# Kernel optimization log

Measured on AMD Instinct MI355X. Metric: run time of the kernel, lower is better.

## Reference

```python
import jax, jax.numpy as jnp
import numpy as np

B, H, W, C = 4, 64, 64, 256
DQK = C // 16  # query/key channels = 16


def setup_inputs() -> dict:
    key = jax.random.key(0)
    ks = jax.random.split(key, 8)
    s = 0.05
    return {
        "x": jax.random.normal(ks[0], (B, H, W, C), dtype=jnp.float32),
        "wq": jax.random.normal(ks[1], (C, DQK), dtype=jnp.float32) * s,
        "bq": jax.random.normal(ks[2], (DQK,), dtype=jnp.float32) * s,
        "wk": jax.random.normal(ks[3], (C, DQK), dtype=jnp.float32) * s,
        "bk": jax.random.normal(ks[4], (DQK,), dtype=jnp.float32) * s,
        "wv": jax.random.normal(ks[5], (C, C), dtype=jnp.float32) * s,
        "bv": jax.random.normal(ks[6], (C,), dtype=jnp.float32) * s,
        "gamma": jax.random.normal(ks[7], (), dtype=jnp.float32),
    }


def reference(x, wq, bq, wk, bk, wv, bv, gamma):
    # 1x1 convs == per-pixel linear projections
    q = jnp.einsum('bhwc,cd->bhwd', x, wq) + bq          # [B,H,W,DQK]
    k = jnp.einsum('bhwc,cd->bhwd', x, wk) + bk          # [B,H,W,DQK]
    v = jnp.einsum('bhwc,cd->bhwd', x, wv) + bv          # [B,H,W,C]
    hw = H * W
    q = q.reshape(B, hw, DQK)
    k = k.reshape(B, hw, DQK)
    v = v.reshape(B, hw, C)
    energy = jnp.einsum('bnd,bmd->bnm', q, k)            # [B,HW,HW]
    attention = jax.nn.softmax(energy, axis=-1)
    out = jnp.einsum('bnm,bmc->bnc', attention, v)       # [B,HW,C]
    out = out.reshape(B, H, W, C)
    return out * gamma + x, attention
```

## Files before the change

kernel.cpp:

```cpp
#include <hip/hip_runtime.h>

typedef _Float16 half8 __attribute__((ext_vector_type(8)));
typedef _Float16 half4v __attribute__((ext_vector_type(4)));
typedef __fp16 fp16x2 __attribute__((ext_vector_type(2)));
typedef float f32x16 __attribute__((ext_vector_type(16)));
typedef float f32x4 __attribute__((ext_vector_type(4)));
typedef unsigned int uint2v __attribute__((ext_vector_type(2)));

#define MFMA16(a, b, c) __builtin_amdgcn_mfma_f32_32x32x16_f16((a), (b), (c), 0, 0, 0)
#define QSC 1.44269504088896f

#define OFF_WB   0
#define OFF_WQK  131072
#define OFF_QF   147456
#define OFF_KF   671744
#define OFF_VB   1196032
#define OFF_MLP  9584640

__device__ inline unsigned int pkf16(float a, float b) {
    union { fp16x2 h; unsigned int u; } cv;
    cv.h = __builtin_amdgcn_cvt_pkrtz(a, b);
    return cv.u;
}
__device__ inline half8 mk8(unsigned int w0, unsigned int w1, unsigned int w2, unsigned int w3) {
    union { unsigned int u[4]; half8 h; } cv;
    cv.u[0] = w0; cv.u[1] = w1; cv.u[2] = w2; cv.u[3] = w3; return cv.h;
}

__global__ __launch_bounds__(256) void k_prep(const float* __restrict__ wq,
                                              const float* __restrict__ wk,
                                              const float* __restrict__ wv,
                                              _Float16* __restrict__ WB,
                                              _Float16* __restrict__ WQK) {
    int idx = blockIdx.x * 256 + threadIdx.x;
    if (idx < 65536) {
        int j = idx & 7, l = (idx >> 3) & 63, kc = idx >> 12;
        int ct = (idx >> 9) & 7;
        int k = kc * 16 + (l >> 5) * 8 + j;
        int c = ct * 32 + (l & 31);
        WB[idx] = (_Float16)wv[k * 256 + c];
    } else if (idx < 65536 + 8192) {
        int t = idx - 65536;
        int j = t & 7, l = (t >> 3) & 63, kc = t >> 9;
        int k = kc * 16 + (l >> 5) * 8 + j;
        int c = l & 31;
        WQK[t] = (_Float16)((c < 16) ? wq[k * 16 + c] : wk[k * 16 + (c - 16)]);
    }
}

__global__ __launch_bounds__(256, 2) void k_proj(const float* __restrict__ x,
                                                 const float* __restrict__ bq,
                                                 const float* __restrict__ bk,
                                                 const float* __restrict__ bv,
                                                 const _Float16* __restrict__ WB,
                                                 const _Float16* __restrict__ WQK,
                                                 _Float16* __restrict__ Qf,
                                                 _Float16* __restrict__ Kf,
                                                 _Float16* __restrict__ VB) {
    const int tid = threadIdx.x;
    const int w = tid >> 6, l = tid & 63, lo = l & 31, h = l >> 5;
    const long rowbase = (long)blockIdx.x * 32;
    const float* xp = x + (rowbase + lo) * 256 + h * 8;

    f32x16 acc0 = {}, acc1 = {}, accQK = {};
#pragma unroll
    for (int kc = 0; kc < 16; ++kc) {
        float4 a0 = *(const float4*)(xp + kc * 16);
        float4 a1 = *(const float4*)(xp + kc * 16 + 4);
        half8 xf;
        xf[0] = (_Float16)a0.x; xf[1] = (_Float16)a0.y; xf[2] = (_Float16)a0.z; xf[3] = (_Float16)a0.w;
        xf[4] = (_Float16)a1.x; xf[5] = (_Float16)a1.y; xf[6] = (_Float16)a1.z; xf[7] = (_Float16)a1.w;
        half8 b0 = *(const half8*)(WB + ((kc * 8 + 2 * w) * 64 + l) * 8);
        half8 b1 = *(const half8*)(WB + ((kc * 8 + 2 * w + 1) * 64 + l) * 8);
        acc0 = MFMA16(xf, b0, acc0);
        acc1 = MFMA16(xf, b1, acc1);
        if (w == 0) {
            half8 bqk = *(const half8*)(WQK + (kc * 64 + l) * 8);
            accQK = MFMA16(xf, bqk, accQK);
        }
    }

    const int b = (int)(rowbase >> 12);
    const int k16base = (int)((rowbase & 4095) >> 4);
#pragma unroll
    for (int cti = 0; cti < 2; ++cti) {
        int ct = 2 * w + cti;
        f32x16 acc = cti ? acc1 : acc0;
        float bias = bv[ct * 32 + lo];
#pragma unroll
        for (int g = 0; g < 4; ++g) {
            int K16 = k16base + (g >> 1);
            int lanep = (g & 1) * 32 + lo;
            _Float16* dst = VB + ((((long)b * 256 + K16) * 8 + ct) * 64 + lanep) * 8 + 4 * h;
            half4v pv;
            pv[0] = (_Float16)(acc[4 * g + 0] + bias);
            pv[1] = (_Float16)(acc[4 * g + 1] + bias);
            pv[2] = (_Float16)(acc[4 * g + 2] + bias);
            pv[3] = (_Float16)(acc[4 * g + 3] + bias);
            *(half4v*)dst = pv;
        }
    }
    if (w == 0) {
        float bias = (lo < 16) ? bq[lo] : bk[lo - 16];
#pragma unroll
        for (int r = 0; r < 16; ++r) {
            int kl = (r & 3) + 8 * (r >> 2) + 4 * h;
            long n = rowbase + kl;
            float v = accQK[r] + bias;
            if (lo < 16) Qf[n * 16 + lo] = (_Float16)(v * QSC);
            else         Kf[n * 16 + (lo - 16)] = (_Float16)v;
        }
    }
}

__global__ __launch_bounds__(256, 4) void k_ml(const _Float16* __restrict__ Qf,
                                               const _Float16* __restrict__ Kf,
                                               float2* __restrict__ MLp) {
    const int bid = blockIdx.x;
    const int kh = bid & 1;
    const int qi = bid >> 1;
    const int b = qi >> 7, qt = qi & 127;
    const int tid = threadIdx.x, w = tid >> 6, l = tid & 63, lo = l & 31, h = l >> 5;
    const int qbase = qt * 32;

    half8 qf = *(const half8*)(Qf + (((long)b * 4096 + qbase + lo) << 4) + h * 8);
    const _Float16* Kb = Kf + ((long)b * 4096 << 4);

    float m = -3e38f, lsum = 0.f;
    for (int i = 0; i < 16; ++i) {
        int t = kh * 64 + i * 4 + w;
        half8 kf = *(const half8*)(Kb + ((t * 32 + lo) << 4) + h * 8);
        f32x16 e = MFMA16(kf, qf, (f32x16){});
        float t0 = fmaxf(fmaxf(e[0], e[1]), fmaxf(e[2], e[3]));
        float t1 = fmaxf(fmaxf(e[4], e[5]), fmaxf(e[6], e[7]));
        float t2 = fmaxf(fmaxf(e[8], e[9]), fmaxf(e[10], e[11]));
        float t3 = fmaxf(fmaxf(e[12], e[13]), fmaxf(e[14], e[15]));
        float tmax = fmaxf(fmaxf(t0, t1), fmaxf(t2, t3));
        tmax = fmaxf(tmax, __shfl_xor(tmax, 32));
        if (tmax > m) { lsum *= exp2f(m - tmax); m = tmax; }
        float ss = 0.f;
#pragma unroll
        for (int r = 0; r < 16; ++r) ss += exp2f(e[r] - m);
        lsum += ss;
    }
    lsum += __shfl_xor(lsum, 32);

    __shared__ float sm[4][32];
    __shared__ float sl[4][32];
    if (l < 32) { sm[w][lo] = m; sl[w][lo] = lsum; }
    __syncthreads();
    if (tid < 32) {
        float M = fmaxf(fmaxf(sm[0][tid], sm[1][tid]), fmaxf(sm[2][tid], sm[3][tid]));
        float L = sl[0][tid] * exp2f(sm[0][tid] - M) + sl[1][tid] * exp2f(sm[1][tid] - M) +
                  sl[2][tid] * exp2f(sm[2][tid] - M) + sl[3][tid] * exp2f(sm[3][tid] - M);
        float2 v; v.x = M; v.y = L;
        MLp[(((long)b * 4096 + qbase + tid) << 1) + kh] = v;
    }
}

__global__ __launch_bounds__(256, 4) void k_attn(const float* __restrict__ x,
                                                 const float* __restrict__ gptr,
                                                 const _Float16* __restrict__ Qf,
                                                 const _Float16* __restrict__ Kf,
                                                 const _Float16* __restrict__ VB,
                                                 const float2* __restrict__ MLp,
                                                 float* __restrict__ out0,
                                                 float* __restrict__ attn) {
    const int bid = blockIdx.x;
    const int sp = bid & 1;
    const int qt = (bid >> 1) & 127;
    const int b  = bid >> 8;
    const int tid = threadIdx.x, w = tid >> 6, l = tid & 63, lo = l & 31, h = l >> 5;
    const int qbase = qt * 32;

    half8 qf = *(const half8*)(Qf + (((long)b * 4096 + qbase + lo) << 4) + h * 8);
    const _Float16* Kb = Kf + ((long)b * 4096 << 4);

    const float2* mlrow = MLp + ((long)(b * 4096 + qbase + lo) << 1);
    float2 mla = mlrow[0];
    float2 mlc = mlrow[1];
    float Mrow = fmaxf(mla.x, mlc.x);
    const float S_lane = Mrow + __log2f(mla.y * exp2f(mla.x - Mrow) + mlc.y * exp2f(mlc.x - Mrow));

    const _Float16* vb = VB + (long)b * 256 * 8 * 64 * 8;

    __shared__ float ldsS[32 * 132];

    const int srow = tid >> 3;
    const int st7 = tid & 7;
    float* aout = attn + (long)b * 4096 * 4096 + ((long)(qbase + srow) << 12) + st7 * 4;

    f32x16 oacc[4] = {};

    for (int i = 0; i < 32; ++i) {
        int t = i * 4 + w;
        half8 kf = *(const half8*)(Kb + ((t * 32 + lo) << 4) + h * 8);
        f32x16 e = MFMA16(kf, qf, (f32x16){});
        float p[16];
#pragma unroll
        for (int r = 0; r < 16; ++r) p[r] = exp2f(e[r] - S_lane);

        if ((i >> 4) == sp) {
            __syncthreads();
#pragma unroll
            for (int g = 0; g < 4; ++g) {
                f32x4 st = { p[4 * g + 0], p[4 * g + 1], p[4 * g + 2], p[4 * g + 3] };
                *(f32x4*)&ldsS[lo * 132 + w * 32 + g * 8 + h * 4] = st;
            }
            __syncthreads();
            float* ap = aout + i * 128;
#pragma unroll
            for (int seg = 0; seg < 4; ++seg) {
                f32x4 v = *(const f32x4*)&ldsS[srow * 132 + seg * 32 + st7 * 4];
                *(f32x4*)(ap + seg * 32) = v;
            }
        }

        unsigned int u0 = pkf16(p[0], p[1]),   x0 = pkf16(p[4], p[5]);
        unsigned int v0 = pkf16(p[2], p[3]),   y0 = pkf16(p[6], p[7]);
        unsigned int u1 = pkf16(p[8], p[9]),   x1 = pkf16(p[12], p[13]);
        unsigned int v1 = pkf16(p[10], p[11]), y1 = pkf16(p[14], p[15]);
        uint2v t0 = __builtin_amdgcn_permlane32_swap(u0, x0, false, false);
        uint2v t1 = __builtin_amdgcn_permlane32_swap(v0, y0, false, false);
        uint2v t2 = __builtin_amdgcn_permlane32_swap(u1, x1, false, false);
        uint2v t3 = __builtin_amdgcn_permlane32_swap(v1, y1, false, false);
        half8 pa0 = mk8(t0.x, t1.x, t0.y, t1.y);
        half8 pa1 = mk8(t2.x, t3.x, t2.y, t3.y);

#pragma unroll
        for (int ct = 0; ct < 4; ++ct) {
            int ctg = 4 * sp + ct;
            half8 vf0 = *(const half8*)(vb + (((long)(2 * t + 0) * 8 + ctg) * 64 + l) * 8);
            half8 vf1 = *(const half8*)(vb + (((long)(2 * t + 1) * 8 + ctg) * 64 + l) * 8);
            oacc[ct] = MFMA16(pa0, vf0, oacc[ct]);
            oacc[ct] = MFMA16(pa1, vf1, oacc[ct]);
        }
    }

#pragma unroll 1
    for (int ww = 0; ww < 4; ++ww) {
        __syncthreads();
        if (w == ww) {
#pragma unroll
            for (int ct = 0; ct < 4; ++ct) {
#pragma unroll
                for (int r = 0; r < 16; ++r) {
                    int row = (r & 3) + 8 * (r >> 2) + 4 * h;
                    float val = oacc[ct][r];
                    if (ww == 0) ldsS[row * 132 + ct * 32 + lo] = val;
                    else         ldsS[row * 132 + ct * 32 + lo] += val;
                }
            }
        }
    }
    __syncthreads();

    float gamma = *gptr;
    int cb = st7 << 4;
    long base = ((long)b * 4096 + qbase + srow) * 256 + sp * 128 + cb;
    const float* xp = x + base;
    float* op = out0 + base;
#pragma unroll
    for (int c0 = 0; c0 < 16; c0 += 4) {
        float4 xv = *(const float4*)(xp + c0);
        f32x4 ov;
        ov.x = gamma * ldsS[srow * 132 + cb + c0 + 0] + xv.x;
        ov.y = gamma * ldsS[srow * 132 + cb + c0 + 1] + xv.y;
        ov.z = gamma * ldsS[srow * 132 + cb + c0 + 2] + xv.z;
        ov.w = gamma * ldsS[srow * 132 + cb + c0 + 3] + xv.w;
        *(f32x4*)(op + c0) = ov;
    }
}

extern "C" void kernel_launch(void* const* d_in, const int* in_sizes, int n_in,
                              void* d_out, int out_size, void* d_ws, size_t ws_size,
                              hipStream_t stream) {
    const float* x  = (const float*)d_in[0];
    const float* wq = (const float*)d_in[1];
    const float* bq = (const float*)d_in[2];
    const float* wk = (const float*)d_in[3];
    const float* bk = (const float*)d_in[4];
    const float* wv = (const float*)d_in[5];
    const float* bv = (const float*)d_in[6];
    const float* gamma = (const float*)d_in[7];

    char* ws = (char*)d_ws;
    _Float16* WB  = (_Float16*)(ws + OFF_WB);
    _Float16* WQK = (_Float16*)(ws + OFF_WQK);
    _Float16* Qf  = (_Float16*)(ws + OFF_QF);
    _Float16* Kf  = (_Float16*)(ws + OFF_KF);
    _Float16* VB  = (_Float16*)(ws + OFF_VB);
    float2*   MLp = (float2*)(ws + OFF_MLP);

    float* out0 = (float*)d_out;
    float* attn = (float*)d_out + 4194304;

    k_prep<<<288, 256, 0, stream>>>(wq, wk, wv, WB, WQK);
    k_proj<<<512, 256, 0, stream>>>(x, bq, bk, bv, WB, WQK, Qf, Kf, VB);
    k_ml  <<<1024, 256, 0, stream>>>(Qf, Kf, MLp);
    k_attn<<<1024, 256, 0, stream>>>(x, gamma, Qf, Kf, VB, MLp, out0, attn);
}
```

Baseline: 144.7 us.

## Fuse softmax stats with PV into one kernel, split attention-matrix write into own kernel

Merges the max/sum pass and the P·V accumulation into a single kernel. Each block now covers all keys and all 256 output channels for 32 queries. It writes the log-sum-exp per row to workspace instead of partial (max, sum) pairs. The large fp32 attention-matrix store moves to a separate, high-occupancy kernel that recomputes QK^T and exp and streams rows out. This separates the compute-heavy PV work from the bandwidth-bound write so each kernel can be shaped for its own bottleneck, at the cost of a third QK^T evaluation, fewer blocks in the PV kernel (512 with 8 accumulators) and lower occupancy there.

```diff
diff --git a/kernel.cpp b/kernel.cpp
--- a/kernel.cpp
+++ b/kernel.cpp
@@ -15,7 +15,7 @@
 #define OFF_QF   147456
 #define OFF_KF   671744
 #define OFF_VB   1196032
-#define OFF_MLP  9584640
+#define OFF_S    9584640
 
 __device__ inline unsigned int pkf16(float a, float b) {
     union { fp16x2 h; unsigned int u; } cv;
@@ -113,13 +113,15 @@
     }
 }
 
-__global__ __launch_bounds__(256, 4) void k_ml(const _Float16* __restrict__ Qf,
-                                               const _Float16* __restrict__ Kf,
-                                               float2* __restrict__ MLp) {
+__global__ __launch_bounds__(256, 2) void k_mlpv(const float* __restrict__ x,
+                                                 const float* __restrict__ gptr,
+                                                 const _Float16* __restrict__ Qf,
+                                                 const _Float16* __restrict__ Kf,
+                                                 const _Float16* __restrict__ VB,
+                                                 float* __restrict__ Sg,
+                                                 float* __restrict__ out0) {
     const int bid = blockIdx.x;
-    const int kh = bid & 1;
-    const int qi = bid >> 1;
-    const int b = qi >> 7, qt = qi & 127;
+    const int b = bid >> 7, qt = bid & 127;
     const int tid = threadIdx.x, w = tid >> 6, l = tid & 63, lo = l & 31, h = l >> 5;
     const int qbase = qt * 32;
 
@@ -127,8 +129,8 @@
     const _Float16* Kb = Kf + ((long)b * 4096 << 4);
 
     float m = -3e38f, lsum = 0.f;
-    for (int i = 0; i < 16; ++i) {
-        int t = kh * 64 + i * 4 + w;
+    for (int i = 0; i < 32; ++i) {
+        int t = i * 4 + w;
         half8 kf = *(const half8*)(Kb + ((t * 32 + lo) << 4) + h * 8);
         f32x16 e = MFMA16(kf, qf, (f32x16){});
         float t0 = fmaxf(fmaxf(e[0], e[1]), fmaxf(e[2], e[3]));
@@ -149,48 +151,19 @@
     __shared__ float sl[4][32];
     if (l < 32) { sm[w][lo] = m; sl[w][lo] = lsum; }
     __syncthreads();
+    float M = fmaxf(fmaxf(sm[0][lo], sm[1][lo]), fmaxf(sm[2][lo], sm[3][lo]));
+    float L = sl[0][lo] * exp2f(sm[0][lo] - M) + sl[1][lo] * exp2f(sm[1][lo] - M) +
+              sl[2][lo] * exp2f(sm[2][lo] - M) + sl[3][lo] * exp2f(sm[3][lo] - M);
+    const float S_lane = M + __log2f(L);
     if (tid < 32) {
-        float M = fmaxf(fmaxf(sm[0][tid], sm[1][tid]), fmaxf(sm[2][tid], sm[3][tid]));
-        float L = sl[0][tid] * exp2f(sm[0][tid] - M) + sl[1][tid] * exp2f(sm[1][tid] - M) +
-                  sl[2][tid] * exp2f(sm[2][tid] - M) + sl[3][tid] * exp2f(sm[3][tid] - M);
-        float2 v; v.x = M; v.y = L;
-        MLp[(((long)b * 4096 + qbase + tid) << 1) + kh] = v;
-    }
-}
-
-__global__ __launch_bounds__(256, 4) void k_attn(const float* __restrict__ x,
-                                                 const float* __restrict__ gptr,
-                                                 const _Float16* __restrict__ Qf,
-                                                 const _Float16* __restrict__ Kf,
-                                                 const _Float16* __restrict__ VB,
-                                                 const float2* __restrict__ MLp,
-                                                 float* __restrict__ out0,
-                                                 float* __restrict__ attn) {
-    const int bid = blockIdx.x;
-    const int sp = bid & 1;
-    const int qt = (bid >> 1) & 127;
-    const int b  = bid >> 8;
-    const int tid = threadIdx.x, w = tid >> 6, l = tid & 63, lo = l & 31, h = l >> 5;
-    const int qbase = qt * 32;
-
-    half8 qf = *(const half8*)(Qf + (((long)b * 4096 + qbase + lo) << 4) + h * 8);
-    const _Float16* Kb = Kf + ((long)b * 4096 << 4);
-
-    const float2* mlrow = MLp + ((long)(b * 4096 + qbase + lo) << 1);
-    float2 mla = mlrow[0];
-    float2 mlc = mlrow[1];
-    float Mrow = fmaxf(mla.x, mlc.x);
-    const float S_lane = Mrow + __log2f(mla.y * exp2f(mla.x - Mrow) + mlc.y * exp2f(mlc.x - Mrow));
+        float Mr = fmaxf(fmaxf(sm[0][tid], sm[1][tid]), fmaxf(sm[2][tid], sm[3][tid]));
+        float Lr = sl[0][tid] * exp2f(sm[0][tid] - Mr) + sl[1][tid] * exp2f(sm[1][tid] - Mr) +
+                   sl[2][tid] * exp2f(sm[2][tid] - Mr) + sl[3][tid] * exp2f(sm[3][tid] - Mr);
+        Sg[b * 4096 + qbase + tid] = Mr + __log2f(Lr);
+    }
 
     const _Float16* vb = VB + (long)b * 256 * 8 * 64 * 8;
-
-    __shared__ float ldsS[32 * 132];
-
-    const int srow = tid >> 3;
-    const int st7 = tid & 7;
-    float* aout = attn + (long)b * 4096 * 4096 + ((long)(qbase + srow) << 12) + st7 * 4;
-
-    f32x16 oacc[4] = {};
+    f32x16 oacc[8] = {};
 
     for (int i = 0; i < 32; ++i) {
         int t = i * 4 + w;
@@ -199,22 +172,6 @@
         float p[16];
 #pragma unroll
         for (int r = 0; r < 16; ++r) p[r] = exp2f(e[r] - S_lane);
-
-        if ((i >> 4) == sp) {
-            __syncthreads();
-#pragma unroll
-            for (int g = 0; g < 4; ++g) {
-                f32x4 st = { p[4 * g + 0], p[4 * g + 1], p[4 * g + 2], p[4 * g + 3] };
-                *(f32x4*)&ldsS[lo * 132 + w * 32 + g * 8 + h * 4] = st;
-            }
-            __syncthreads();
-            float* ap = aout + i * 128;
-#pragma unroll
-            for (int seg = 0; seg < 4; ++seg) {
-                f32x4 v = *(const f32x4*)&ldsS[srow * 132 + seg * 32 + st7 * 4];
-                *(f32x4*)(ap + seg * 32) = v;
-            }
-        }
 
         unsigned int u0 = pkf16(p[0], p[1]),   x0 = pkf16(p[4], p[5]);
         unsigned int v0 = pkf16(p[2], p[3]),   y0 = pkf16(p[6], p[7]);
@@ -228,27 +185,27 @@
         half8 pa1 = mk8(t2.x, t3.x, t2.y, t3.y);
 
 #pragma unroll
-        for (int ct = 0; ct < 4; ++ct) {
-            int ctg = 4 * sp + ct;
-            half8 vf0 = *(const half8*)(vb + (((long)(2 * t + 0) * 8 + ctg) * 64 + l) * 8);
-            half8 vf1 = *(const half8*)(vb + (((long)(2 * t + 1) * 8 + ctg) * 64 + l) * 8);
+        for (int ct = 0; ct < 8; ++ct) {
+            half8 vf0 = *(const half8*)(vb + (((long)(2 * t + 0) * 8 + ct) * 64 + l) * 8);
+            half8 vf1 = *(const half8*)(vb + (((long)(2 * t + 1) * 8 + ct) * 64 + l) * 8);
             oacc[ct] = MFMA16(pa0, vf0, oacc[ct]);
             oacc[ct] = MFMA16(pa1, vf1, oacc[ct]);
         }
     }
 
+    __shared__ float ldsO[32 * 260];
 #pragma unroll 1
     for (int ww = 0; ww < 4; ++ww) {
         __syncthreads();
         if (w == ww) {
 #pragma unroll
-            for (int ct = 0; ct < 4; ++ct) {
+            for (int ct = 0; ct < 8; ++ct) {
 #pragma unroll
                 for (int r = 0; r < 16; ++r) {
                     int row = (r & 3) + 8 * (r >> 2) + 4 * h;
                     float val = oacc[ct][r];
-                    if (ww == 0) ldsS[row * 132 + ct * 32 + lo] = val;
-                    else         ldsS[row * 132 + ct * 32 + lo] += val;
+                    if (ww == 0) ldsO[row * 260 + ct * 32 + lo] = val;
+                    else         ldsO[row * 260 + ct * 32 + lo] += val;
                 }
             }
         }
@@ -256,19 +213,65 @@
     __syncthreads();
 
     float gamma = *gptr;
-    int cb = st7 << 4;
-    long base = ((long)b * 4096 + qbase + srow) * 256 + sp * 128 + cb;
+    int row = tid >> 3;
+    int cb = (tid & 7) << 5;
+    long base = ((long)b * 4096 + qbase + row) * 256 + cb;
     const float* xp = x + base;
     float* op = out0 + base;
 #pragma unroll
-    for (int c0 = 0; c0 < 16; c0 += 4) {
+    for (int c0 = 0; c0 < 32; c0 += 4) {
         float4 xv = *(const float4*)(xp + c0);
         f32x4 ov;
-        ov.x = gamma * ldsS[srow * 132 + cb + c0 + 0] + xv.x;
-        ov.y = gamma * ldsS[srow * 132 + cb + c0 + 1] + xv.y;
-        ov.z = gamma * ldsS[srow * 132 + cb + c0 + 2] + xv.z;
-        ov.w = gamma * ldsS[srow * 132 + cb + c0 + 3] + xv.w;
+        ov.x = gamma * ldsO[row * 260 + cb + c0 + 0] + xv.x;
+        ov.y = gamma * ldsO[row * 260 + cb + c0 + 1] + xv.y;
+        ov.z = gamma * ldsO[row * 260 + cb + c0 + 2] + xv.z;
+        ov.w = gamma * ldsO[row * 260 + cb + c0 + 3] + xv.w;
         *(f32x4*)(op + c0) = ov;
+    }
+}
+
+__global__ __launch_bounds__(256, 8) void k_awr(const _Float16* __restrict__ Qf,
+                                                const _Float16* __restrict__ Kf,
+                                                const float* __restrict__ Sg,
+                                                float* __restrict__ attn) {
+    const int bid = blockIdx.x;
+    const int kq = bid & 3;
+    const int qt = (bid >> 2) & 127;
+    const int b  = bid >> 9;
+    const int tid = threadIdx.x, kw = tid >> 6, l = tid & 63, lo = l & 31, h = l >> 5;
+    const int qbase = qt * 32;
+
+    half8 qf = *(const half8*)(Qf + (((long)b * 4096 + qbase + lo) << 4) + h * 8);
+    const _Float16* Kb = Kf + ((long)b * 4096 << 4);
+    const float S_lane = Sg[b * 4096 + qbase + lo];
+
+    __shared__ float ldsS[32 * 132];
+
+    const int srow = tid >> 3, st7 = tid & 7;
+    float* aout = attn + (long)b * 4096 * 4096 + ((long)(qbase + srow) << 12)
+                + kq * 1024 + st7 * 4;
+
+#pragma unroll 1
+    for (int i = 0; i < 8; ++i) {
+        int t = kq * 32 + i * 4 + kw;
+        half8 kf = *(const half8*)(Kb + ((t * 32 + lo) << 4) + h * 8);
+        f32x16 e = MFMA16(kf, qf, (f32x16){});
+
+        __syncthreads();
+#pragma unroll
+        for (int g = 0; g < 4; ++g) {
+            f32x4 st = { exp2f(e[4 * g + 0] - S_lane), exp2f(e[4 * g + 1] - S_lane),
+                         exp2f(e[4 * g + 2] - S_lane), exp2f(e[4 * g + 3] - S_lane) };
+            *(f32x4*)&ldsS[lo * 132 + kw * 32 + g * 8 + h * 4] = st;
+        }
+        __syncthreads();
+
+        float* ap = aout + i * 128;
+#pragma unroll
+        for (int seg = 0; seg < 4; ++seg) {
+            f32x4 v = *(const f32x4*)&ldsS[srow * 132 + seg * 32 + st7 * 4];
+            *(f32x4*)(ap + seg * 32) = v;
+        }
     }
 }
 
@@ -290,13 +293,13 @@
     _Float16* Qf  = (_Float16*)(ws + OFF_QF);
     _Float16* Kf  = (_Float16*)(ws + OFF_KF);
     _Float16* VB  = (_Float16*)(ws + OFF_VB);
-    float2*   MLp = (float2*)(ws + OFF_MLP);
+    float*    Sg  = (float*)(ws + OFF_S);
 
     float* out0 = (float*)d_out;
     float* attn = (float*)d_out + 4194304;
 
     k_prep<<<288, 256, 0, stream>>>(wq, wk, wv, WB, WQK);
     k_proj<<<512, 256, 0, stream>>>(x, bq, bk, bv, WB, WQK, Qf, Kf, VB);
-    k_ml  <<<1024, 256, 0, stream>>>(Qf, Kf, MLp);
-    k_attn<<<1024, 256, 0, stream>>>(x, gamma, Qf, Kf, VB, MLp, out0, attn);
-}
+    k_mlpv<<<512, 256, 0, stream>>>(x, gamma, Qf, Kf, VB, Sg, out0);
+    k_awr <<<2048, 256, 0, stream>>>(Qf, Kf, Sg, attn);
+}
```

Measured after the change: 177.3 us. 1.23x slower.
